# Optimization experiments

Hardware: AMD Instinct MI355X
Metric: run time of the kernel (lower is better)

## Reference

```python
import jax, jax.numpy as jnp
import numpy as np

NUM_CLASSES = 20
FC = 512  # feature_channels
H = W = 28


def _conv(x, w, b):
    y = jax.lax.conv_general_dilated(x, w, (1, 1), 'SAME',
                                     dimension_numbers=('NCHW', 'OIHW', 'NCHW'))
    return y + b[None, :, None, None]


def _center_map(centers, height, width):
    # centers: [B, N, 4] = (x, y, class, conf); vectorized scatter replacing the python loop
    B, N, _ = centers.shape
    xp = (centers[..., 0] * width).astype(jnp.int32)   # int() truncation; x>=0 so == floor
    yp = (centers[..., 1] * height).astype(jnp.int32)
    conf = centers[..., 3]
    valid = (xp >= 0) & (xp < width) & (yp >= 0) & (yp < height)
    flat = jnp.where(valid, yp * width + xp, height * width)  # invalid -> dummy slot
    m = jnp.zeros((B, height * width + 1), centers.dtype)
    m = m.at[jnp.arange(B)[:, None], flat].set(conf)
    return m[:, :height * width].reshape(B, 1, height, width)


def setup_inputs() -> dict:
    key = jax.random.key(0)
    ks = jax.random.split(key, 16)
    B = 256
    image = jax.random.normal(ks[0], (B, 3, H, W), jnp.float32)
    features = jax.random.normal(ks[1], (B, FC, 7, 7), jnp.float32)
    centers = jax.random.uniform(ks[2], (B, 100, 4), jnp.float32)

    def conv_w(k, co, ci):
        s = 1.0 / np.sqrt(ci * 9)
        return jax.random.uniform(k, (co, ci, 3, 3), jnp.float32, -s, s)

    def lin_w(k, co, ci):
        s = 1.0 / np.sqrt(ci)
        return jax.random.uniform(k, (co, ci), jnp.float32, -s, s)

    cin = FC + 3 + 1  # 516
    return {
        'image': image, 'features': features, 'centers': centers,
        'w1': conv_w(ks[3], 128, cin), 'b1': jnp.zeros((128,), jnp.float32),
        'w2': conv_w(ks[4], 64, 128), 'b2': jnp.zeros((64,), jnp.float32),
        'w3': conv_w(ks[5], 32, 64), 'b3': jnp.zeros((32,), jnp.float32),
        'w4': conv_w(ks[6], 16, 32), 'b4': jnp.zeros((16,), jnp.float32),
        'fw1': lin_w(ks[7], 256, 16 * H * W), 'fb1': jnp.zeros((256,), jnp.float32),
        'fw2': lin_w(ks[8], 4 + NUM_CLASSES, 256), 'fb2': jnp.zeros((4 + NUM_CLASSES,), jnp.float32),
    }


def reference(image, features, centers, w1, b1, w2, b2, w3, b3, w4, b4, fw1, fb1, fw2, fb2):
    B = image.shape[0]
    feats = jax.image.resize(features, (B, FC, H, W), method='bilinear')  # align_corners=False
    cmap = _center_map(centers, H, W)
    x = jnp.concatenate([image, feats, cmap], axis=1)  # [B, 516, 28, 28]
    x = jax.nn.relu(_conv(x, w1, b1))
    x = jax.nn.relu(_conv(x, w2, b2))
    x = jax.nn.relu(_conv(x, w3, b3))
    x = jax.nn.relu(_conv(x, w4, b4))
    x = x.reshape(B, -1)
    x = jax.nn.relu(x @ fw1.T + fb1)
    action = x @ fw2.T + fb2  # [B, 4 + num_classes]
    action = action.at[:, 2].set(jax.nn.sigmoid(action[:, 2]))
    action = action.at[:, 3].set(jax.nn.sigmoid(action[:, 3]))
    return action
```

## Files before the change

### kernel.cpp

```cpp
#include <hip/hip_runtime.h>

typedef _Float16 f16;
typedef _Float16 f16x8 __attribute__((ext_vector_type(8)));
typedef float    f32x4 __attribute__((ext_vector_type(4)));

static __device__ __forceinline__ f16x8 ld8(const f16* p) {
    return *reinterpret_cast<const f16x8*>(p);
}

static constexpr size_t W1T_B  = 1253376;
static constexpr size_t W2T_B  = 147456;
static constexpr size_t W3T_B  = 36864;
static constexpr size_t W4T_B  = 9216;
static constexpr size_t FW1T_B = 6422528;
static constexpr size_t WEIGHTS_B = W1T_B + W2T_B + W3T_B + W4T_B + FW1T_B;

static constexpr size_t PB_X0 = 979200;
static constexpr size_t PB_X1 = 230400;
static constexpr size_t PB_X2 = 115200;
static constexpr size_t PB_X3 = 57600;
static constexpr size_t PB_X4 = 25088;
static constexpr size_t PB_X5 = 512;
static constexpr size_t PER_BATCH = PB_X0 + PB_X1 + PB_X2 + PB_X3 + PB_X4 + PB_X5;

static __device__ __forceinline__ void wxf(const float* __restrict__ w, f16* __restrict__ wt,
                                           int i, int CINr, int NCB, int COUT) {
    int co = i % COUT;
    int r  = i / COUT;
    int hi = r & 3; r >>= 2;
    int cb = r % NCB;
    int tap = r / NCB;
    f16x8 v;
    #pragma unroll
    for (int j = 0; j < 8; ++j) {
        int ci = cb * 32 + hi * 8 + j;
        float x = (ci < CINr) ? w[((size_t)co * CINr + ci) * 9 + tap] : 0.f;
        v[j] = (f16)x;
    }
    *reinterpret_cast<f16x8*>(wt + (size_t)i * 8) = v;
}

static constexpr int S1 = 9 * 17 * 4 * 128;
static constexpr int S2 = 9 * 4  * 4 * 64;
static constexpr int S3 = 9 * 2  * 4 * 32;
static constexpr int S4 = 9 * 1  * 4 * 16;
static constexpr int SW = S1 + S2 + S3 + S4;
static constexpr int SFW = 256 * 12544;
static constexpr int PREP_TOT = SW + SFW;

__global__ void prep_all(const float* __restrict__ w1, const float* __restrict__ w2,
                         const float* __restrict__ w3, const float* __restrict__ w4,
                         const float* __restrict__ fw1,
                         f16* __restrict__ W1t, f16* __restrict__ W2t,
                         f16* __restrict__ W3t, f16* __restrict__ W4t,
                         f16* __restrict__ FW1t) {
    int t = blockIdx.x * 256 + threadIdx.x;
    if (t >= PREP_TOT) return;
    if (t < S1) { wxf(w1, W1t, t, 516, 17, 128); return; }
    t -= S1;
    if (t < S2) { wxf(w2, W2t, t, 128, 4, 64); return; }
    t -= S2;
    if (t < S3) { wxf(w3, W3t, t, 64, 2, 32); return; }
    t -= S3;
    if (t < S4) { wxf(w4, W4t, t, 32, 1, 16); return; }
    t -= S4;
    int o = t / 12544, idx = t % 12544;
    int y = idx / 448, rem = idx % 448;
    int x = rem / 16, c = rem & 15;
    FW1t[t] = (f16)fw1[(size_t)o * 12544 + c * 784 + y * 28 + x];
}

static __device__ __forceinline__ void ring_yx(int bi, int& y, int& x) {
    if (bi < 30)      { y = 0;        x = bi; }
    else if (bi < 60) { y = 29;       x = bi - 30; }
    else if (bi < 88) { y = bi - 59;  x = 0; }
    else              { y = bi - 87;  x = 29; }
}

__global__ __launch_bounds__(512) void build_x0(
        const float* __restrict__ img, const float* __restrict__ feat,
        const float* __restrict__ centers,
        f16* __restrict__ X0, f16* __restrict__ X1,
        f16* __restrict__ X2, f16* __restrict__ X3, int b0) {
    const int bl = blockIdx.x;
    const int b  = b0 + bl;
    const int tid = threadIdx.x;
    f16* x0b = X0 + (size_t)bl * (30 * 30 * 544);

    for (int i = tid; i < 116 * 544; i += 512) {
        int c = i % 544, bi = i / 544;
        int y, x; ring_yx(bi, y, x);
        x0b[((size_t)y * 30 + x) * 544 + c] = (f16)0.f;
    }
    for (int i = tid; i < 784; i += 512) {
        int y = i / 28, x = i % 28;
        x0b[((size_t)(y + 1) * 30 + x + 1) * 544 + 515] = (f16)0.f;
    }
    for (int i = tid; i < 3 * 784; i += 512) {
        int c = i / 784, p = i % 784;
        int y = p / 28, x = p % 28;
        x0b[((size_t)(y + 1) * 30 + x + 1) * 544 + c] =
            (f16)img[((size_t)b * 3 + c) * 784 + p];
    }
    {
        const float* fb = feat + ((size_t)b * 512 + tid) * 49;
        float r0[7], r1[7];
        int cur = -100;
        for (int y = 0; y < 28; ++y) {
            float sy = (y + 0.5f) * 0.25f - 0.5f;
            float fy = floorf(sy);
            int iy0 = (int)fy;
            float wy1 = sy - fy, wy0 = 1.f - wy1;
            if (iy0 != cur) {
                cur = iy0;
                int i0 = iy0 < 0 ? 0 : iy0;
                int i1 = (iy0 + 1 > 6) ? 6 : iy0 + 1;
                #pragma unroll
                for (int j = 0; j < 7; ++j) { r0[j] = fb[i0 * 7 + j]; r1[j] = fb[i1 * 7 + j]; }
            }
            f16* orow = x0b + ((size_t)(y + 1) * 30 + 1) * 544 + 3 + tid;
            #pragma unroll 28
            for (int x = 0; x < 28; ++x) {
                float sx = (x + 0.5f) * 0.25f - 0.5f;
                float fx = floorf(sx);
                int ix0 = (int)fx;
                float wx1 = sx - fx, wx0 = 1.f - wx1;
                int j0 = ix0 < 0 ? 0 : ix0;
                int j1 = (ix0 + 1 > 6) ? 6 : ix0 + 1;
                float v = wy0 * (wx0 * r0[j0] + wx1 * r0[j1]) +
                          wy1 * (wx0 * r1[j0] + wx1 * r1[j1]);
                orow[(size_t)x * 544] = (f16)v;
            }
        }
    }
    {
        f16* x1b = X1 + (size_t)bl * (30 * 30 * 128);
        for (int i = tid; i < 116 * 128; i += 512) {
            int c = i % 128, bi = i / 128;
            int y, x; ring_yx(bi, y, x);
            x1b[((size_t)y * 30 + x) * 128 + c] = (f16)0.f;
        }
        f16* x2b = X2 + (size_t)bl * (30 * 30 * 64);
        for (int i = tid; i < 116 * 64; i += 512) {
            int c = i % 64, bi = i / 64;
            int y, x; ring_yx(bi, y, x);
            x2b[((size_t)y * 30 + x) * 64 + c] = (f16)0.f;
        }
        f16* x3b = X3 + (size_t)bl * (30 * 30 * 32);
        for (int i = tid; i < 116 * 32; i += 512) {
            int c = i % 32, bi = i / 32;
            int y, x; ring_yx(bi, y, x);
            x3b[((size_t)y * 30 + x) * 32 + c] = (f16)0.f;
        }
    }
    __syncthreads();
    if (tid == 0) {
        const float* cb = centers + (size_t)b * 400;
        for (int n = 0; n < 100; ++n) {
            float cx = cb[n * 4 + 0], cy = cb[n * 4 + 1], conf = cb[n * 4 + 3];
            int xp = (int)(cx * 28.f);
            int yp = (int)(cy * 28.f);
            if (xp >= 0 && xp < 28 && yp >= 0 && yp < 28)
                x0b[((size_t)(yp + 1) * 30 + xp + 1) * 544 + 515] = (f16)conf;
        }
    }
}

template<int CIN, int COUT, int GM, int GN, int WNT, int MW, bool PADOUT>
__global__ __launch_bounds__(512) void conv3x3(const f16* __restrict__ Xin,
                                               const f16* __restrict__ Wt,
                                               const float* __restrict__ bias,
                                               f16* __restrict__ Xout) {
    constexpr int NCB  = CIN / 32;
    constexpr int NV_B = 9 * 4 * COUT;
    constexpr int NV_A = 10 * 30 * 4;
    __shared__ f16 Bs[NV_B * 8];
    __shared__ f16 As[NV_A * 8];

    const int rg = blockIdx.x;
    const int b  = blockIdx.y;
    const int tid = threadIdx.x;
    const int wave = tid >> 6;
    const int lane = tid & 63;
    const int lm = lane & 15, hi = lane >> 4;
    const int wm = wave % GM, wn = wave / GM;
    const int MT = (rg < 3) ? 14 : 7;

    f32x4 acc[MW][WNT];
    #pragma unroll
    for (int k = 0; k < MW; ++k)
        #pragma unroll
        for (int n = 0; n < WNT; ++n)
            acc[k][n] = (f32x4){0.f, 0.f, 0.f, 0.f};

    int lrow0[MW], lcol0[MW];
    #pragma unroll
    for (int k = 0; k < MW; ++k) {
        const int m = wm + k * GM;
        const int p = m * 16 + lm;
        lrow0[k] = p / 28;
        lcol0[k] = p - lrow0[k] * 28;
    }

    for (int cb = 0; cb < NCB; ++cb) {
        for (int v = tid; v < NV_B; v += 512) {
            const int tap = v / (4 * COUT);
            const int w   = v - tap * (4 * COUT);
            *reinterpret_cast<f16x8*>(Bs + (size_t)v * 8) =
                ld8(Wt + ((size_t)(tap * NCB + cb) * (4 * COUT) + w) * 8);
        }
        for (int v = tid; v < NV_A; v += 512) {
            const int c8  = v & 3;
            const int r2  = v >> 2;
            const int px  = r2 % 30;
            const int row = r2 / 30;
            const int grow = rg * 8 + row;
            if (grow < 30) {
                *reinterpret_cast<f16x8*>(As + ((size_t)(c8 * 10 + row) * 30 + px) * 8) =
                    ld8(Xin + ((size_t)(b * 30 + grow) * 30 + px) * CIN + cb * 32 + c8 * 8);
            }
        }
        __syncthreads();

        #pragma unroll
        for (int tap = 0; tap < 9; ++tap) {
            f16x8 bf[WNT];
            #pragma unroll
            for (int n = 0; n < WNT; ++n)
                bf[n] = *reinterpret_cast<const f16x8*>(
                    Bs + ((size_t)(tap * 4 + hi) * COUT + (wn * WNT + n) * 16 + lm) * 8);
            const int dy = tap / 3, dx = tap - dy * 3;
            #pragma unroll
            for (int k = 0; k < MW; ++k) {
                if (wm + k * GM < MT) {
                    const f16x8 af = *reinterpret_cast<const f16x8*>(
                        As + ((size_t)(hi * 10 + lrow0[k] + dy) * 30 + lcol0[k] + dx) * 8);
                    #pragma unroll
                    for (int n = 0; n < WNT; ++n)
                        acc[k][n] = __builtin_amdgcn_mfma_f32_16x16x32_f16(af, bf[n], acc[k][n], 0, 0, 0);
                }
            }
        }
        __syncthreads();
    }

    #pragma unroll
    for (int k = 0; k < MW; ++k) {
        const int m = wm + k * GM;
        if (m < MT) {
            #pragma unroll
            for (int n = 0; n < WNT; ++n) {
                const int co = (wn * WNT + n) * 16 + lm;
                const float bv = bias[co];
                #pragma unroll
                for (int r = 0; r < 4; ++r) {
                    const int p = m * 16 + hi * 4 + r;
                    const int yl = p / 28, x = p - yl * 28;
                    const float v = fmaxf(acc[k][n][r] + bv, 0.f);
                    size_t off;
                    if (PADOUT)
                        off = ((size_t)(b * 30 + rg * 8 + yl + 1) * 30 + (x + 1)) * COUT + co;
                    else
                        off = ((size_t)b * 784 + (rg * 8 + yl) * 28 + x) * COUT + co;
                    Xout[off] = (f16)v;
                }
            }
        }
    }
}

__global__ __launch_bounds__(256) void fc1k(const f16* __restrict__ X4,
                                            const f16* __restrict__ FW1t,
                                            const float* __restrict__ fb1,
                                            f16* __restrict__ X5, int CH) {
    const int bm = blockIdx.x;
    const int nt = blockIdx.y * 4 + (threadIdx.x >> 6);
    const int lane = threadIdx.x & 63;
    const int lm = lane & 15, hi = lane >> 4;
    f32x4 acc = (f32x4){0.f, 0.f, 0.f, 0.f};
    const int row0 = bm * 16 + lm;
    const int rowA = (row0 < CH) ? row0 : 0;
    const f16* arow = X4 + (size_t)rowA * 12544;
    const int o = nt * 16 + lm;
    const f16* brow = FW1t + (size_t)o * 12544;
    for (int kk = 0; kk < 12544; kk += 32) {
        const f16x8 af = ld8(arow + kk + hi * 8);
        const f16x8 bf = ld8(brow + kk + hi * 8);
        acc = __builtin_amdgcn_mfma_f32_16x16x32_f16(af, bf, acc, 0, 0, 0);
    }
    const float bv = fb1[o];
    #pragma unroll
    for (int r = 0; r < 4; ++r) {
        const int row = bm * 16 + hi * 4 + r;
        if (row < CH)
            X5[(size_t)row * 256 + o] = (f16)fmaxf(acc[r] + bv, 0.f);
    }
}

__global__ void fc2k(const f16* __restrict__ X5, const float* __restrict__ fw2,
                     const float* __restrict__ fb2, float* __restrict__ out, int CH) {
    int t = blockIdx.x * 256 + threadIdx.x;
    if (t < CH * 24) {
        int b = t / 24, o = t % 24;
        float s = fb2[o];
        const f16* xr = X5 + (size_t)b * 256;
        const float* wr = fw2 + (size_t)o * 256;
        for (int k = 0; k < 256; ++k) s += (float)xr[k] * wr[k];
        if (o == 2 || o == 3) s = 1.f / (1.f + expf(-s));
        out[t] = s;
    }
}

extern "C" void kernel_launch(void* const* d_in, const int* in_sizes, int n_in,
                              void* d_out, int out_size, void* d_ws, size_t ws_size,
                              hipStream_t stream) {
    const float* image    = (const float*)d_in[0];
    const float* features = (const float*)d_in[1];
    const float* centers  = (const float*)d_in[2];
    const float* w1  = (const float*)d_in[3];
    const float* b1  = (const float*)d_in[4];
    const float* w2  = (const float*)d_in[5];
    const float* b2  = (const float*)d_in[6];
    const float* w3  = (const float*)d_in[7];
    const float* b3  = (const float*)d_in[8];
    const float* w4  = (const float*)d_in[9];
    const float* b4  = (const float*)d_in[10];
    const float* fw1 = (const float*)d_in[11];
    const float* fb1 = (const float*)d_in[12];
    const float* fw2 = (const float*)d_in[13];
    const float* fb2 = (const float*)d_in[14];

    int CH = 8;
    for (int c = 256; c >= 8; c >>= 1) {
        if (WEIGHTS_B + (size_t)c * PER_BATCH <= ws_size) { CH = c; break; }
    }

    char* ws = (char*)d_ws;
    f16* W1t  = (f16*)(ws);
    f16* W2t  = (f16*)(ws + W1T_B);
    f16* W3t  = (f16*)(ws + W1T_B + W2T_B);
    f16* W4t  = (f16*)(ws + W1T_B + W2T_B + W3T_B);
    f16* FW1t = (f16*)(ws + W1T_B + W2T_B + W3T_B + W4T_B);
    char* act = ws + WEIGHTS_B;
    f16* X0 = (f16*)(act);
    f16* X1 = (f16*)(act + (size_t)CH * PB_X0);
    f16* X2 = (f16*)(act + (size_t)CH * (PB_X0 + PB_X1));
    f16* X3 = (f16*)(act + (size_t)CH * (PB_X0 + PB_X1 + PB_X2));
    f16* X4 = (f16*)(act + (size_t)CH * (PB_X0 + PB_X1 + PB_X2 + PB_X3));
    f16* X5 = (f16*)(act + (size_t)CH * (PB_X0 + PB_X1 + PB_X2 + PB_X3 + PB_X4));

    prep_all<<<(PREP_TOT + 255) / 256, 256, 0, stream>>>(w1, w2, w3, w4, fw1,
                                                         W1t, W2t, W3t, W4t, FW1t);

    for (int b0 = 0; b0 < 256; b0 += CH) {
        build_x0<<<CH, 512, 0, stream>>>(image, features, centers,
                                         X0, X1, X2, X3, b0);

        dim3 cgrid(4, CH);
        conv3x3<544, 128, 4, 2, 4, 4, true ><<<cgrid, 512, 0, stream>>>(X0, W1t, b1, X1);
        conv3x3<128, 64,  4, 2, 2, 4, true ><<<cgrid, 512, 0, stream>>>(X1, W2t, b2, X2);
        conv3x3<64,  32,  4, 2, 1, 4, true ><<<cgrid, 512, 0, stream>>>(X2, W3t, b3, X3);
        conv3x3<32,  16,  8, 1, 1, 2, false><<<cgrid, 512, 0, stream>>>(X3, W4t, b4, X4);

        dim3 fgrid((CH + 15) / 16, 4);
        fc1k<<<fgrid, 256, 0, stream>>>(X4, FW1t, fb1, X5, CH);
        fc2k<<<(CH * 24 + 255) / 256, 256, 0, stream>>>(X5, fw2, fb2,
                                                        (float*)d_out + (size_t)b0 * 24, CH);
    }
}
```

Baseline: 918.6 us.

## Replace first conv with 4-wave kernel reading activations directly from global

Adds a new conv3x3_w4 kernel for the first 544->128 convolution. It uses 256 threads and a 7x CH grid, with each block covering 4 output rows (112 pixels). Weights for each channel block are staged in LDS, while activation fragments are loaded straight from global memory instead of through a shared-memory tile. The aim is to raise block count and occupancy and cut LDS traffic and syncs, at the cost of more global and L2 reads of the input.

Measured after the change: 1.267 ms. 37.9% more time.

```diff
diff --git a/kernel.cpp b/kernel.cpp
--- a/kernel.cpp
+++ b/kernel.cpp
@@ -166,6 +166,89 @@
     }
 }
 
+template<int CIN, int COUT, bool PADOUT>
+__global__ __launch_bounds__(256) void conv3x3_w4(const f16* __restrict__ Xin,
+                                                  const f16* __restrict__ Wt,
+                                                  const float* __restrict__ bias,
+                                                  f16* __restrict__ Xout) {
+    constexpr int NCB  = CIN / 32;
+    constexpr int WNT  = COUT / 64;
+    constexpr int NV_B = 9 * 4 * COUT;
+    __shared__ f16 Bs[NV_B * 8];
+
+    const int rg = blockIdx.x;
+    const int b  = blockIdx.y;
+    const int tid = threadIdx.x;
+    const int wn = tid >> 6;
+    const int lane = tid & 63;
+    const int lm = lane & 15, hi = lane >> 4;
+
+    f32x4 acc[7][WNT];
+    #pragma unroll
+    for (int k = 0; k < 7; ++k)
+        #pragma unroll
+        for (int n = 0; n < WNT; ++n)
+            acc[k][n] = (f32x4){0.f, 0.f, 0.f, 0.f};
+
+    int inoff[7];
+    #pragma unroll
+    for (int k = 0; k < 7; ++k) {
+        const int p = k * 16 + lm;
+        const int yl = p / 28, x = p - yl * 28;
+        inoff[k] = ((b * 30 + rg * 4 + yl) * 30 + x) * CIN;
+    }
+
+    for (int cb = 0; cb < NCB; ++cb) {
+        for (int v = tid; v < NV_B; v += 256) {
+            const int tap = v / (4 * COUT);
+            const int w   = v - tap * (4 * COUT);
+            *reinterpret_cast<f16x8*>(Bs + (size_t)v * 8) =
+                ld8(Wt + ((size_t)(tap * NCB + cb) * (4 * COUT) + w) * 8);
+        }
+        __syncthreads();
+
+        #pragma unroll
+        for (int tap = 0; tap < 9; ++tap) {
+            f16x8 bf[WNT];
+            #pragma unroll
+            for (int n = 0; n < WNT; ++n)
+                bf[n] = *reinterpret_cast<const f16x8*>(
+                    Bs + ((size_t)(tap * 4 + hi) * COUT + (wn * WNT + n) * 16 + lm) * 8);
+            const int dy = tap / 3, dx = tap - dy * 3;
+            const int dOff = (dy * 30 + dx) * CIN + cb * 32 + hi * 8;
+            #pragma unroll
+            for (int k = 0; k < 7; ++k) {
+                const f16x8 af = ld8(Xin + inoff[k] + dOff);
+                #pragma unroll
+                for (int n = 0; n < WNT; ++n)
+                    acc[k][n] = __builtin_amdgcn_mfma_f32_16x16x32_f16(af, bf[n], acc[k][n], 0, 0, 0);
+            }
+        }
+        __syncthreads();
+    }
+
+    #pragma unroll
+    for (int k = 0; k < 7; ++k) {
+        #pragma unroll
+        for (int n = 0; n < WNT; ++n) {
+            const int co = (wn * WNT + n) * 16 + lm;
+            const float bv = bias[co];
+            #pragma unroll
+            for (int r = 0; r < 4; ++r) {
+                const int p = k * 16 + hi * 4 + r;
+                const int yl = p / 28, x = p - yl * 28;
+                const float v = fmaxf(acc[k][n][r] + bv, 0.f);
+                size_t off;
+                if (PADOUT)
+                    off = ((size_t)(b * 30 + rg * 4 + yl + 1) * 30 + (x + 1)) * COUT + co;
+                else
+                    off = ((size_t)b * 784 + (rg * 4 + yl) * 28 + x) * COUT + co;
+                Xout[off] = (f16)v;
+            }
+        }
+    }
+}
+
 template<int CIN, int COUT, int GM, int GN, int WNT, int MW, bool PADOUT>
 __global__ __launch_bounds__(512) void conv3x3(const f16* __restrict__ Xin,
                                                const f16* __restrict__ Wt,
@@ -356,8 +439,9 @@
         build_x0<<<CH, 512, 0, stream>>>(image, features, centers,
                                          X0, X1, X2, X3, b0);
 
+        conv3x3_w4<544, 128, true><<<dim3(7, CH), 256, 0, stream>>>(X0, W1t, b1, X1);
+
         dim3 cgrid(4, CH);
-        conv3x3<544, 128, 4, 2, 4, 4, true ><<<cgrid, 512, 0, stream>>>(X0, W1t, b1, X1);
         conv3x3<128, 64,  4, 2, 2, 4, true ><<<cgrid, 512, 0, stream>>>(X1, W2t, b2, X2);
         conv3x3<64,  32,  4, 2, 1, 4, true ><<<cgrid, 512, 0, stream>>>(X2, W3t, b3, X3);
         conv3x3<32,  16,  8, 1, 1, 2, false><<<cgrid, 512, 0, stream>>>(X3, W4t, b4, X4);
```
